# Performance work log

Hardware: AMD Instinct MI355X
Metric: run time of the kernel (lower is better)

## Reference

```python
import jax, jax.numpy as jnp
import numpy as np

B, S, D = 32, 512, 512      # batch, seq_len, d_model
H, K = 16, 32               # head_num, head_dim
A = 256                     # attention_hidden_dim


def setup_inputs() -> dict:
    key = jax.random.key(0)
    ks = jax.random.split(key, 10)
    s = lambda fan_in: 1.0 / np.sqrt(fan_in)
    return {
        "x":   jax.random.normal(ks[0], (B, S, D), dtype=jnp.float32),
        # per-head Q projections: Linear(D, D), stored [H, in, out]
        "Qw":  jax.random.normal(ks[1], (H, D, D), dtype=jnp.float32) * s(D),
        "Qb":  jax.random.normal(ks[2], (H, D), dtype=jnp.float32) * s(D),
        # per-head V projections: Linear(D, K)
        "Vw":  jax.random.normal(ks[3], (H, D, K), dtype=jnp.float32) * s(D),
        "Vb":  jax.random.normal(ks[4], (H, K), dtype=jnp.float32) * s(D),
        # additive attention pooling: Linear(H*K, A) then Linear(A, 1)
        "Wv":  jax.random.normal(ks[5], (H * K, A), dtype=jnp.float32) * s(H * K),
        "bv":  jax.random.normal(ks[6], (A,), dtype=jnp.float32) * s(H * K),
        "wq":  jax.random.normal(ks[7], (A, 1), dtype=jnp.float32) * s(A),
        "bq":  jax.random.normal(ks[8], (1,), dtype=jnp.float32) * s(A),
    }


def reference(x, Qw, Qb, Vw, Vb, Wv, bv, wq, bq):
    # per-head query projection: [B, H, S, D]
    q = jnp.einsum("bsd,hde->bhse", x, Qw) + Qb[None, :, None, :]
    # raw scores: [B, H, S, S] (s = query pos, t = key pos)
    scores = jnp.einsum("bhse,bte->bhst", q, x)
    # NOTE: softmax over dim=-2 (the QUERY axis), not the usual key axis
    attn = jax.nn.softmax(scores, axis=-2)
    # context: [B, H, S, D]
    ctx = jnp.einsum("bhst,btd->bhsd", attn, x)
    # per-head value projection then concat heads -> [B, S, H*K]
    head_out = jnp.einsum("bhsd,hdk->bshk", ctx, Vw) + Vb[None, None, :, :]
    h = head_out.reshape(B, S, H * K)
    # dropout is identity at inference
    # additive attention pooling
    a = jnp.tanh(h @ Wv + bv) @ wq + bq          # [B, S, 1]
    z = jnp.einsum("bs,bsk->bk", a[..., 0], h)   # [B, H*K]
    return z
```

## Files before the change

kernel.cpp:

```cpp
#include <hip/hip_runtime.h>

#define DEVFN __device__ __forceinline__

typedef _Float16 f16;
typedef _Float16 f16x8 __attribute__((ext_vector_type(8)));
typedef _Float16 f16x4 __attribute__((ext_vector_type(4)));
typedef float    f32x4 __attribute__((ext_vector_type(4)));

enum { NB = 32, NS = 512, ND = 512, NH = 16, NK = 32, NA = 256 };

#define SZ(x) ((size_t)(x))

typedef __attribute__((address_space(3))) void       as3_void;
typedef const __attribute__((address_space(1))) void as1_cvoid;
DEVFN void ldsdma16(const void* g, void* l) {
  __builtin_amdgcn_global_load_lds((as1_cvoid*)g, (as3_void*)l, 16, 0, 0);
}

DEVFN void gemm_core_128(const f16* __restrict__ Ag, const f16* __restrict__ Bg,
                         int lda, int ldb, int nk, f16* lds, f32x4 acc[4][4]) {
  f16* As = lds;
  f16* Bs = lds + 128 * 64;
  const int tid  = threadIdx.x;
  const int lane = tid & 63;
  const int wvid = tid >> 6, wr = wvid >> 1, wc = wvid & 1;
  const int srow = tid >> 3, scol = (tid & 7) * 8;
  const int frow = lane & 15, fk = (lane >> 4) * 8;
  for (int ks = 0; ks < nk; ++ks) {
    const f16* ga = Ag + ks * 64 + scol;
    const f16* gb = Bg + ks * 64 + scol;
#pragma unroll
    for (int r = 0; r < 4; ++r) {
      ldsdma16(ga + SZ(r * 32 + srow) * lda, As + SZ(r * 32 + srow) * 64 + scol);
      ldsdma16(gb + SZ(r * 32 + srow) * ldb, Bs + SZ(r * 32 + srow) * 64 + scol);
    }
    __syncthreads();
#pragma unroll
    for (int kk = 0; kk < 64; kk += 32) {
      f16x8 a[4], b[4];
#pragma unroll
      for (int i = 0; i < 4; ++i)
        a[i] = *(const f16x8*)(As + SZ(wr * 64 + i * 16 + frow) * 64 + kk + fk);
#pragma unroll
      for (int j = 0; j < 4; ++j)
        b[j] = *(const f16x8*)(Bs + SZ(wc * 64 + j * 16 + frow) * 64 + kk + fk);
#pragma unroll
      for (int i = 0; i < 4; ++i)
#pragma unroll
        for (int j = 0; j < 4; ++j)
          acc[i][j] = __builtin_amdgcn_mfma_f32_16x16x32_f16(a[i], b[j], acc[i][j], 0, 0, 0);
    }
    __syncthreads();
  }
}

DEVFN void wlds_write(f16* wlds, int row, int col, f16 v) {
  int byte = (row * 256 + col * 2) ^ ((row & 7) << 4);
  *(f16*)((char*)wlds + byte) = v;
}
DEVFN f16x8 wlds_read8(const f16* wlds, int row, int col ) {
  int byte = (row * 256 + col * 2) ^ ((row & 7) << 4);
  return *(const f16x8*)((const char*)wlds + byte);
}

__global__ __launch_bounds__(256) void k_cast4(const float* __restrict__ s,
                                               f16* __restrict__ d, int n4) {
  int i = blockIdx.x * 256 + threadIdx.x;
  if (i >= n4) return;
  float4 v = ((const float4*)s)[i];
  f16x4 o; o[0] = (f16)v.x; o[1] = (f16)v.y; o[2] = (f16)v.z; o[3] = (f16)v.w;
  ((f16x4*)d)[i] = o;
}

__global__ void k_tcast(const float* __restrict__ src, f16* __restrict__ dst,
                        int R, int C, long sStride, long dStride) {
  __shared__ float tile[32][33];
  src += (long)blockIdx.z * sStride;
  dst += (long)blockIdx.z * dStride;
  int c0 = blockIdx.x * 32, r0 = blockIdx.y * 32;
  int tx = threadIdx.x, ty = threadIdx.y;
#pragma unroll
  for (int i = 0; i < 4; ++i)
    tile[ty + 8 * i][tx] = src[(long)(r0 + ty + 8 * i) * C + c0 + tx];
  __syncthreads();
#pragma unroll
  for (int i = 0; i < 4; ++i)
    dst[(long)(c0 + ty + 8 * i) * R + r0 + tx] = (f16)tile[tx][ty + 8 * i];
}

__global__ __launch_bounds__(256) void k_gemm_xv(const f16* __restrict__ xh,
                                                 const f16* __restrict__ vwt,
                                                 f16* __restrict__ xvt) {
  __shared__ f16 smem[128 * 64 * 2];
  int z = blockIdx.z, b = z >> 2, hg = z & 3, tm = blockIdx.x;
  f32x4 acc[4][4] = {};
  gemm_core_128(xh + SZ(b) * NS * ND + SZ(tm) * 128 * ND,
                vwt + SZ(hg) * 4 * NK * ND, ND, ND, ND / 64, smem, acc);
  int tid = threadIdx.x, lane = tid & 63, wvid = tid >> 6, wr = wvid >> 1, wc = wvid & 1;
  int rbase = (lane >> 4) * 4, cbase = lane & 15;
#pragma unroll
  for (int mi = 0; mi < 4; ++mi)
#pragma unroll
    for (int ni = 0; ni < 4; ++ni) {
      int n = wc * 64 + ni * 16 + cbase;
      int hh = hg * 4 + (n >> 5), kk = n & 31;
#pragma unroll
      for (int r = 0; r < 4; ++r) {
        int t = tm * 128 + wr * 64 + mi * 16 + rbase + r;
        xvt[(SZ(b * NH + hh) * NK + kk) * NS + t] = (f16)acc[mi][ni][r];
      }
    }
}

__global__ __launch_bounds__(256) void k_gemm_q(const f16* __restrict__ xh,
                                                const f16* __restrict__ qwt,
                                                const float* __restrict__ Qb,
                                                f16* __restrict__ qc, int b0) {
  __shared__ f16 smem[128 * 64 * 2];
  int bhl = blockIdx.z, b = b0 + (bhl >> 4), h = bhl & 15;
  int tm = blockIdx.x, tn = blockIdx.y;
  f32x4 acc[4][4] = {};
  gemm_core_128(xh + SZ(b) * NS * ND + SZ(tm) * 128 * ND,
                qwt + SZ(h) * ND * ND + SZ(tn) * 128 * ND, ND, ND, ND / 64, smem, acc);
  int tid = threadIdx.x, lane = tid & 63, wvid = tid >> 6, wr = wvid >> 1, wc = wvid & 1;
  int rbase = (lane >> 4) * 4, cbase = lane & 15;
  f16* qb = qc + SZ(bhl) * NS * ND;
#pragma unroll
  for (int mi = 0; mi < 4; ++mi)
#pragma unroll
    for (int ni = 0; ni < 4; ++ni) {
      int colg = tn * 128 + wc * 64 + ni * 16 + cbase;
      float bias = Qb[h * ND + colg];
#pragma unroll
      for (int r = 0; r < 4; ++r) {
        int rowg = tm * 128 + wr * 64 + mi * 16 + rbase + r;
        qb[SZ(rowg) * ND + colg] = (f16)(acc[mi][ni][r] + bias);
      }
    }
}

__global__ __launch_bounds__(256) void k_scores_stats(const f16* __restrict__ qc,
                                                      const f16* __restrict__ xh,
                                                      f16* __restrict__ sc,
                                                      float* __restrict__ mp,
                                                      float* __restrict__ zp, int b0) {
  __shared__ f16 smem[128 * 64 * 2];
  int bhl = blockIdx.z, b = b0 + (bhl >> 4);
  int st = blockIdx.x, tt = blockIdx.y;
  f32x4 acc[4][4] = {};
  gemm_core_128(qc + SZ(bhl) * NS * ND + SZ(st) * 128 * ND,
                xh + SZ(b) * NS * ND + SZ(tt) * 128 * ND, ND, ND, ND / 64, smem, acc);
  int tid = threadIdx.x, lane = tid & 63, wvid = tid >> 6, wr = wvid >> 1, wc = wvid & 1;
  f16* scb = sc + (SZ(bhl * 4 + st) * 4 + tt) * (128 * 128);
#pragma unroll
  for (int mi = 0; mi < 4; ++mi)
#pragma unroll
    for (int ni = 0; ni < 4; ++ni) {
      f16x4 o;
#pragma unroll
      for (int r = 0; r < 4; ++r) o[r] = (f16)acc[mi][ni][r];
      ((f16x4*)(scb + (mi * 4 + ni) * 1024))[tid] = o;
    }
  float mx[4], sm[4];
#pragma unroll
  for (int ni = 0; ni < 4; ++ni) {
    float m = -1e30f;
#pragma unroll
    for (int mi = 0; mi < 4; ++mi)
#pragma unroll
      for (int r = 0; r < 4; ++r) m = fmaxf(m, acc[mi][ni][r]);
    m = fmaxf(m, __shfl_xor(m, 16));
    m = fmaxf(m, __shfl_xor(m, 32));
    float s = 0.f;
#pragma unroll
    for (int mi = 0; mi < 4; ++mi)
#pragma unroll
      for (int r = 0; r < 4; ++r) s += __expf(acc[mi][ni][r] - m);
    s += __shfl_xor(s, 16);
    s += __shfl_xor(s, 32);
    mx[ni] = m; sm[ni] = s;
  }
  float2* sbuf = (float2*)smem;
  if (lane < 16) {
#pragma unroll
    for (int ni = 0; ni < 4; ++ni)
      sbuf[wr * 128 + wc * 64 + ni * 16 + lane] = make_float2(mx[ni], sm[ni]);
  }
  __syncthreads();
  if (tid < 128) {
    float2 p0 = sbuf[tid], p1 = sbuf[128 + tid];
    float m = fmaxf(p0.x, p1.x);
    float zz = p0.y * __expf(p0.x - m) + p1.y * __expf(p1.x - m);
    size_t idx = (SZ(bhl) * 4 + st) * NS + tt * 128 + tid;
    mp[idx] = m; zp[idx] = zz;
  }
}

__global__ __launch_bounds__(256) void k_stats_combine(const float* __restrict__ mp,
                                                       const float* __restrict__ zp,
                                                       float* __restrict__ mf,
                                                       float* __restrict__ rz) {
  int i = blockIdx.x * 256 + threadIdx.x;
  int bhl = i >> 9, t = i & (NS - 1);
  float mv[4], m = -1e30f;
#pragma unroll
  for (int st = 0; st < 4; ++st) {
    mv[st] = mp[(SZ(bhl) * 4 + st) * NS + t];
    m = fmaxf(m, mv[st]);
  }
  float z = 0.f;
#pragma unroll
  for (int st = 0; st < 4; ++st) z += zp[(SZ(bhl) * 4 + st) * NS + t] * __expf(mv[st] - m);
  mf[i] = m; rz[i] = 1.0f / z;
}

__global__ __launch_bounds__(256) void k_norm_pv(const f16* __restrict__ sc,
                                                 const f16* __restrict__ xvt,
                                                 const float* __restrict__ mf,
                                                 const float* __restrict__ rz,
                                                 const float* __restrict__ Vb,
                                                 f16* __restrict__ h16, int b0) {
  __shared__ f16 wlds[128 * 128];
  int bhl = blockIdx.y, b = b0 + (bhl >> 4), h = bhl & 15;
  int st = blockIdx.x;
  int tid = threadIdx.x, lane = tid & 63, wvid = tid >> 6, wr = wvid >> 1, wc = wvid & 1;
  int rbase = (lane >> 4) * 4, cbase = lane & 15, fk = (lane >> 4) * 8;
  f32x4 acc2[2][2] = {};
  const f16* xvh = xvt + SZ(b * NH + h) * NK * NS;
  for (int tt = 0; tt < 4; ++tt) {
    const f16* scb = sc + (SZ(bhl * 4 + st) * 4 + tt) * (128 * 128);
#pragma unroll
    for (int ni = 0; ni < 4; ++ni) {
      int tl = wc * 64 + ni * 16 + cbase;
      int tg = tt * 128 + tl;
      float mv = mf[SZ(bhl) * NS + tg], rzv = rz[SZ(bhl) * NS + tg];
#pragma unroll
      for (int mi = 0; mi < 4; ++mi) {
        f16x4 v = ((const f16x4*)(scb + (mi * 4 + ni) * 1024))[tid];
#pragma unroll
        for (int r = 0; r < 4; ++r) {
          int sl = wr * 64 + mi * 16 + rbase + r;
          wlds_write(wlds, sl, tl, (f16)(__expf((float)v[r] - mv) * rzv));
        }
      }
    }
    __syncthreads();
    const f16* xvb = xvh + tt * 128;
#pragma unroll
    for (int tc = 0; tc < 4; ++tc) {
      f16x8 aw[2], bx[2];
#pragma unroll
      for (int m2 = 0; m2 < 2; ++m2)
        aw[m2] = wlds_read8(wlds, wvid * 32 + m2 * 16 + cbase, tc * 32 + fk);
#pragma unroll
      for (int n2 = 0; n2 < 2; ++n2)
        bx[n2] = *(const f16x8*)(xvb + SZ(n2 * 16 + cbase) * NS + tc * 32 + fk);
#pragma unroll
      for (int m2 = 0; m2 < 2; ++m2)
#pragma unroll
        for (int n2 = 0; n2 < 2; ++n2)
          acc2[m2][n2] = __builtin_amdgcn_mfma_f32_16x16x32_f16(aw[m2], bx[n2], acc2[m2][n2], 0, 0, 0);
    }
    __syncthreads();
  }
  const float* vb = Vb + h * NK;
#pragma unroll
  for (int m2 = 0; m2 < 2; ++m2)
#pragma unroll
    for (int n2 = 0; n2 < 2; ++n2)
#pragma unroll
      for (int r = 0; r < 4; ++r) {
        int sg = st * 128 + wvid * 32 + m2 * 16 + rbase + r;
        int kk = n2 * 16 + cbase;
        float val = acc2[m2][n2][r] + vb[kk];
        h16[SZ(b * NS + sg) * (NH * NK) + h * NK + kk] = (f16)val;
      }
}

__global__ __launch_bounds__(256) void k_gemm_u(const f16* __restrict__ h16,
                                                const f16* __restrict__ wvt,
                                                const float* __restrict__ bv,
                                                f16* __restrict__ U) {
  __shared__ f16 smem[128 * 64 * 2];
  int tm = blockIdx.x, tn = blockIdx.y;
  f32x4 acc[4][4] = {};
  gemm_core_128(h16 + SZ(tm) * 128 * ND, wvt + SZ(tn) * 128 * ND, ND, ND, ND / 64, smem, acc);
  int tid = threadIdx.x, lane = tid & 63, wvid = tid >> 6, wr = wvid >> 1, wc = wvid & 1;
  int rbase = (lane >> 4) * 4, cbase = lane & 15;
#pragma unroll
  for (int mi = 0; mi < 4; ++mi)
#pragma unroll
    for (int ni = 0; ni < 4; ++ni) {
      int colg = tn * 128 + wc * 64 + ni * 16 + cbase;
      float bias = bv[colg];
#pragma unroll
      for (int r = 0; r < 4; ++r) {
        int rowg = tm * 128 + wr * 64 + mi * 16 + rbase + r;
        U[SZ(rowg) * NA + colg] = (f16)tanhf(acc[mi][ni][r] + bias);
      }
    }
}

__global__ __launch_bounds__(256) void k_a(const f16* __restrict__ U,
                                           const float* __restrict__ wq,
                                           const float* __restrict__ bq,
                                           float* __restrict__ a) {
  int wid = (blockIdx.x * 256 + threadIdx.x) >> 6;
  int lane = threadIdx.x & 63;
  const f16* u = U + SZ(wid) * NA;
  float p = 0.f;
#pragma unroll
  for (int j = 0; j < NA / 64; ++j) p += (float)u[lane + 64 * j] * wq[lane + 64 * j];
#pragma unroll
  for (int o = 32; o; o >>= 1) p += __shfl_xor(p, o);
  if (lane == 0) a[wid] = p + bq[0];
}

__global__ __launch_bounds__(256) void k_zpart(const f16* __restrict__ h16,
                                               const float* __restrict__ a,
                                               float* __restrict__ zpt) {
  int b = blockIdx.y, c = blockIdx.x, tid = threadIdx.x;
  float z0 = 0.f, z1 = 0.f;
  for (int s = 0; s < 64; ++s) {
    int sg = c * 64 + s;
    float av = a[b * NS + sg];
    const f16* hr = h16 + SZ(b * NS + sg) * (NH * NK);
    z0 += av * (float)hr[tid];
    z1 += av * (float)hr[tid + 256];
  }
  zpt[SZ(b * 8 + c) * 512 + tid] = z0;
  zpt[SZ(b * 8 + c) * 512 + tid + 256] = z1;
}

__global__ __launch_bounds__(256) void k_zred(const float* __restrict__ zpt,
                                              float* __restrict__ out) {
  int i = blockIdx.x * 256 + threadIdx.x;
  int b = i >> 9, k = i & 511;
  float z = 0.f;
#pragma unroll
  for (int c = 0; c < 8; ++c) z += zpt[SZ(b * 8 + c) * 512 + k];
  out[i] = z;
}

static size_t ws_plan(int cb, size_t off[15]) {
  size_t o = 0;
  auto put = [&](size_t bytes) { size_t r = o; o += (bytes + 255) & ~SZ(255); return r; };
  off[0]  = put(SZ(NB) * NS * ND * 2);
  off[1]  = put(SZ(NH) * ND * ND * 2);
  off[2]  = put(SZ(NA) * ND * 2);
  off[3]  = put(SZ(NH) * NK * ND * 2);
  off[4]  = put(SZ(NB) * NH * NK * NS * 2);
  off[5]  = put(SZ(cb) * NH * NS * ND * 2);
  off[6]  = put(SZ(cb) * NH * NS * NS * 2);
  off[7]  = put(SZ(cb) * NH * 4 * NS * 4);
  off[8]  = put(SZ(cb) * NH * 4 * NS * 4);
  off[9]  = put(SZ(cb) * NH * NS * 4);
  off[10] = put(SZ(cb) * NH * NS * 4);
  off[11] = put(SZ(NB) * NS * NH * NK * 2);
  off[12] = put(SZ(NB) * NS * NA * 2);
  off[13] = put(SZ(NB) * NS * 4);
  off[14] = put(SZ(NB) * 8 * NH * NK * 4);
  return o;
}

extern "C" void kernel_launch(void* const* d_in, const int* in_sizes, int n_in,
                              void* d_out, int out_size, void* d_ws, size_t ws_size,
                              hipStream_t stream) {
  const float* x  = (const float*)d_in[0];
  const float* Qw = (const float*)d_in[1];
  const float* Qb = (const float*)d_in[2];
  const float* Vw = (const float*)d_in[3];
  const float* Vb = (const float*)d_in[4];
  const float* Wv = (const float*)d_in[5];
  const float* bv = (const float*)d_in[6];
  const float* wq = (const float*)d_in[7];
  const float* bq = (const float*)d_in[8];

  int cbv = 0;
  size_t off[15];
  const int cand[5] = {32, 16, 8, 4, 2};
  for (int ci = 0; ci < 5; ++ci) {
    if (ws_plan(cand[ci], off) <= ws_size) { cbv = cand[ci]; break; }
  }
  if (cbv == 0) return;

  char* ws = (char*)d_ws;
  f16*   xh   = (f16*)(ws + off[0]);
  f16*   qwt  = (f16*)(ws + off[1]);
  f16*   wvt  = (f16*)(ws + off[2]);
  f16*   vwt  = (f16*)(ws + off[3]);
  f16*   xvt  = (f16*)(ws + off[4]);
  f16*   qc   = (f16*)(ws + off[5]);
  f16*   sc   = (f16*)(ws + off[6]);
  float* mp   = (float*)(ws + off[7]);
  float* zps  = (float*)(ws + off[8]);
  float* mf   = (float*)(ws + off[9]);
  float* rz   = (float*)(ws + off[10]);
  f16*   h16  = (f16*)(ws + off[11]);
  f16*   U    = (f16*)(ws + off[12]);
  float* a    = (float*)(ws + off[13]);
  float* zpt  = (float*)(ws + off[14]);
  float* zout = (float*)d_out;

  k_cast4<<<SZ(NB) * NS * ND / 4 / 256, 256, 0, stream>>>(x, xh, NB * NS * ND / 4);
  k_tcast<<<dim3(16, 16, 16), dim3(32, 8), 0, stream>>>(Qw, qwt, ND, ND, (long)ND * ND, (long)ND * ND);
  k_tcast<<<dim3(8, 16, 1), dim3(32, 8), 0, stream>>>(Wv, wvt, ND, NA, 0, 0);
  k_tcast<<<dim3(1, 16, 16), dim3(32, 8), 0, stream>>>(Vw, vwt, ND, NK, (long)ND * NK, (long)NK * ND);
  k_gemm_xv<<<dim3(4, 1, NB * 4), 256, 0, stream>>>(xh, vwt, xvt);

  for (int b0 = 0; b0 < NB; b0 += cbv) {
    k_gemm_q<<<dim3(4, 4, cbv * NH), 256, 0, stream>>>(xh, qwt, Qb, qc, b0);
    k_scores_stats<<<dim3(4, 4, cbv * NH), 256, 0, stream>>>(qc, xh, sc, mp, zps, b0);
    k_stats_combine<<<cbv * NH * NS / 256, 256, 0, stream>>>(mp, zps, mf, rz);
    k_norm_pv<<<dim3(4, cbv * NH), 256, 0, stream>>>(sc, xvt, mf, rz, Vb, h16, b0);
  }

  k_gemm_u<<<dim3(NB * NS / 128, 2, 1), 256, 0, stream>>>(h16, wvt, bv, U);
  k_a<<<NB * NS / 4, 256, 0, stream>>>(U, wq, bq, a);
  k_zpart<<<dim3(8, NB), 256, 0, stream>>>(h16, a, zpt);
  k_zred<<<NB * 512 / 256, 256, 0, stream>>>(zpt, zout);
}
```

Baseline: 612.9 us.

## Store exponentiated scores, precompute per-tile softmax scales, swizzle blocks across XCDs

The scores kernel now reduces the column max across the tile first, then writes exp(score - tile max) as f16 instead of raw scores. The combine kernel emits one scale per (query tile, key) pair, so the normalize/PV kernel does a single multiply instead of an exp per element. GEMM blocks in the Q and scores kernels are remapped with an XCD-aware swizzle so tiles that share inputs land on the same chiplet's cache, and the z-partial loop reads f16 pairs. This adds an extra barrier and LDS round-trip in the scores kernel. Storing exponentials in f16 instead of raw scores changes rounding behaviour.

```diff
diff --git a/kernel.cpp b/kernel.cpp
--- a/kernel.cpp
+++ b/kernel.cpp
@@ -5,6 +5,7 @@
 typedef _Float16 f16;
 typedef _Float16 f16x8 __attribute__((ext_vector_type(8)));
 typedef _Float16 f16x4 __attribute__((ext_vector_type(4)));
+typedef _Float16 f16x2 __attribute__((ext_vector_type(2)));
 typedef float    f32x4 __attribute__((ext_vector_type(4)));
 
 enum { NB = 32, NS = 512, ND = 512, NH = 16, NK = 32, NA = 256 };
@@ -15,6 +16,10 @@
 typedef const __attribute__((address_space(1))) void as1_cvoid;
 DEVFN void ldsdma16(const void* g, void* l) {
   __builtin_amdgcn_global_load_lds((as1_cvoid*)g, (as3_void*)l, 16, 0, 0);
+}
+
+DEVFN int xcd_swz(int flat, int n) {
+  return (flat & 7) * (n >> 3) + (flat >> 3);
 }
 
 DEVFN void gemm_core_128(const f16* __restrict__ Ag, const f16* __restrict__ Bg,
@@ -117,8 +122,11 @@
                                                 const float* __restrict__ Qb,
                                                 f16* __restrict__ qc, int b0) {
   __shared__ f16 smem[128 * 64 * 2];
-  int bhl = blockIdx.z, b = b0 + (bhl >> 4), h = bhl & 15;
-  int tm = blockIdx.x, tn = blockIdx.y;
+  int n = gridDim.x * gridDim.y * gridDim.z;
+  int flat = blockIdx.x + gridDim.x * (blockIdx.y + gridDim.y * blockIdx.z);
+  int lg = xcd_swz(flat, n);
+  int tm = lg & 3, tn = (lg >> 2) & 3, bhl = lg >> 4;
+  int b = b0 + (bhl >> 4), h = bhl & 15;
   f32x4 acc[4][4] = {};
   gemm_core_128(xh + SZ(b) * NS * ND + SZ(tm) * 128 * ND,
                 qwt + SZ(h) * ND * ND + SZ(tn) * 128 * ND, ND, ND, ND / 64, smem, acc);
@@ -145,23 +153,18 @@
                                                       float* __restrict__ mp,
                                                       float* __restrict__ zp, int b0) {
   __shared__ f16 smem[128 * 64 * 2];
-  int bhl = blockIdx.z, b = b0 + (bhl >> 4);
-  int st = blockIdx.x, tt = blockIdx.y;
+  int n = gridDim.x * gridDim.y * gridDim.z;
+  int flat = blockIdx.x + gridDim.x * (blockIdx.y + gridDim.y * blockIdx.z);
+  int lg = xcd_swz(flat, n);
+  int st = lg & 3, tt = (lg >> 2) & 3, bhl = lg >> 4;
+  int b = b0 + (bhl >> 4);
   f32x4 acc[4][4] = {};
   gemm_core_128(qc + SZ(bhl) * NS * ND + SZ(st) * 128 * ND,
                 xh + SZ(b) * NS * ND + SZ(tt) * 128 * ND, ND, ND, ND / 64, smem, acc);
   int tid = threadIdx.x, lane = tid & 63, wvid = tid >> 6, wr = wvid >> 1, wc = wvid & 1;
-  f16* scb = sc + (SZ(bhl * 4 + st) * 4 + tt) * (128 * 128);
-#pragma unroll
-  for (int mi = 0; mi < 4; ++mi)
-#pragma unroll
-    for (int ni = 0; ni < 4; ++ni) {
-      f16x4 o;
-#pragma unroll
-      for (int r = 0; r < 4; ++r) o[r] = (f16)acc[mi][ni][r];
-      ((f16x4*)(scb + (mi * 4 + ni) * 1024))[tid] = o;
-    }
-  float mx[4], sm[4];
+  float* sbuf = (float*)smem;
+
+  float mh[4];
 #pragma unroll
   for (int ni = 0; ni < 4; ++ni) {
     float m = -1e30f;
@@ -171,26 +174,53 @@
       for (int r = 0; r < 4; ++r) m = fmaxf(m, acc[mi][ni][r]);
     m = fmaxf(m, __shfl_xor(m, 16));
     m = fmaxf(m, __shfl_xor(m, 32));
-    float s = 0.f;
-#pragma unroll
-    for (int mi = 0; mi < 4; ++mi)
-#pragma unroll
-      for (int r = 0; r < 4; ++r) s += __expf(acc[mi][ni][r] - m);
-    s += __shfl_xor(s, 16);
-    s += __shfl_xor(s, 32);
-    mx[ni] = m; sm[ni] = s;
-  }
-  float2* sbuf = (float2*)smem;
+    mh[ni] = m;
+  }
   if (lane < 16) {
 #pragma unroll
     for (int ni = 0; ni < 4; ++ni)
-      sbuf[wr * 128 + wc * 64 + ni * 16 + lane] = make_float2(mx[ni], sm[ni]);
+      sbuf[wr * 128 + wc * 64 + ni * 16 + lane] = mh[ni];
+  }
+  __syncthreads();
+  int cbase = lane & 15;
+  float tmc[4];
+#pragma unroll
+  for (int ni = 0; ni < 4; ++ni) {
+    int col = wc * 64 + ni * 16 + cbase;
+    tmc[ni] = fmaxf(sbuf[col], sbuf[128 + col]);
+  }
+  f16* scb = sc + (SZ(bhl * 4 + st) * 4 + tt) * (128 * 128);
+  float sm[4];
+#pragma unroll
+  for (int ni = 0; ni < 4; ++ni) sm[ni] = 0.f;
+#pragma unroll
+  for (int mi = 0; mi < 4; ++mi) {
+#pragma unroll
+    for (int ni = 0; ni < 4; ++ni) {
+      f16x4 o;
+#pragma unroll
+      for (int r = 0; r < 4; ++r) {
+        float ev = __expf(acc[mi][ni][r] - tmc[ni]);
+        o[r] = (f16)ev;
+        sm[ni] += ev;
+      }
+      ((f16x4*)(scb + (mi * 4 + ni) * 1024))[tid] = o;
+    }
+  }
+#pragma unroll
+  for (int ni = 0; ni < 4; ++ni) {
+    sm[ni] += __shfl_xor(sm[ni], 16);
+    sm[ni] += __shfl_xor(sm[ni], 32);
+  }
+  if (lane < 16) {
+#pragma unroll
+    for (int ni = 0; ni < 4; ++ni)
+      sbuf[256 + wr * 128 + wc * 64 + ni * 16 + lane] = sm[ni];
   }
   __syncthreads();
   if (tid < 128) {
-    float2 p0 = sbuf[tid], p1 = sbuf[128 + tid];
-    float m = fmaxf(p0.x, p1.x);
-    float zz = p0.y * __expf(p0.x - m) + p1.y * __expf(p1.x - m);
+    float m  = fmaxf(sbuf[tid], sbuf[128 + tid]);
+    float zz = sbuf[256 + tid] + sbuf[384 + tid];
     size_t idx = (SZ(bhl) * 4 + st) * NS + tt * 128 + tid;
     mp[idx] = m; zp[idx] = zz;
   }
@@ -198,8 +228,7 @@
 
 __global__ __launch_bounds__(256) void k_stats_combine(const float* __restrict__ mp,
                                                        const float* __restrict__ zp,
-                                                       float* __restrict__ mf,
-                                                       float* __restrict__ rz) {
+                                                       float* __restrict__ cs) {
   int i = blockIdx.x * 256 + threadIdx.x;
   int bhl = i >> 9, t = i & (NS - 1);
   float mv[4], m = -1e30f;
@@ -208,16 +237,21 @@
     mv[st] = mp[(SZ(bhl) * 4 + st) * NS + t];
     m = fmaxf(m, mv[st]);
   }
-  float z = 0.f;
-#pragma unroll
-  for (int st = 0; st < 4; ++st) z += zp[(SZ(bhl) * 4 + st) * NS + t] * __expf(mv[st] - m);
-  mf[i] = m; rz[i] = 1.0f / z;
+  float es[4], Z = 0.f;
+#pragma unroll
+  for (int st = 0; st < 4; ++st) {
+    es[st] = __expf(mv[st] - m);
+    Z += zp[(SZ(bhl) * 4 + st) * NS + t] * es[st];
+  }
+  float rZ = 1.0f / Z;
+#pragma unroll
+  for (int st = 0; st < 4; ++st)
+    cs[(SZ(bhl) * 4 + st) * NS + t] = es[st] * rZ;
 }
 
 __global__ __launch_bounds__(256) void k_norm_pv(const f16* __restrict__ sc,
                                                  const f16* __restrict__ xvt,
-                                                 const float* __restrict__ mf,
-                                                 const float* __restrict__ rz,
+                                                 const float* __restrict__ cs,
                                                  const float* __restrict__ Vb,
                                                  f16* __restrict__ h16, int b0) {
   __shared__ f16 wlds[128 * 128];
@@ -232,15 +266,14 @@
 #pragma unroll
     for (int ni = 0; ni < 4; ++ni) {
       int tl = wc * 64 + ni * 16 + cbase;
-      int tg = tt * 128 + tl;
-      float mv = mf[SZ(bhl) * NS + tg], rzv = rz[SZ(bhl) * NS + tg];
+      float csv = cs[(SZ(bhl) * 4 + st) * NS + tt * 128 + tl];
 #pragma unroll
       for (int mi = 0; mi < 4; ++mi) {
         f16x4 v = ((const f16x4*)(scb + (mi * 4 + ni) * 1024))[tid];
 #pragma unroll
         for (int r = 0; r < 4; ++r) {
           int sl = wr * 64 + mi * 16 + rbase + r;
-          wlds_write(wlds, sl, tl, (f16)(__expf((float)v[r] - mv) * rzv));
+          wlds_write(wlds, sl, tl, (f16)((float)v[r] * csv));
         }
       }
     }
@@ -325,11 +358,12 @@
     int sg = c * 64 + s;
     float av = a[b * NS + sg];
     const f16* hr = h16 + SZ(b * NS + sg) * (NH * NK);
-    z0 += av * (float)hr[tid];
-    z1 += av * (float)hr[tid + 256];
-  }
-  zpt[SZ(b * 8 + c) * 512 + tid] = z0;
-  zpt[SZ(b * 8 + c) * 512 + tid + 256] = z1;
+    f16x2 v = ((const f16x2*)hr)[tid];
+    z0 += av * (float)v[0];
+    z1 += av * (float)v[1];
+  }
+  zpt[SZ(b * 8 + c) * 512 + 2 * tid]     = z0;
+  zpt[SZ(b * 8 + c) * 512 + 2 * tid + 1] = z1;
 }
 
 __global__ __launch_bounds__(256) void k_zred(const float* __restrict__ zpt,
@@ -342,7 +376,7 @@
   out[i] = z;
 }
 
-static size_t ws_plan(int cb, size_t off[15]) {
+static size_t ws_plan(int cb, size_t off[14]) {
   size_t o = 0;
   auto put = [&](size_t bytes) { size_t r = o; o += (bytes + 255) & ~SZ(255); return r; };
   off[0]  = put(SZ(NB) * NS * ND * 2);
@@ -354,12 +388,11 @@
   off[6]  = put(SZ(cb) * NH * NS * NS * 2);
   off[7]  = put(SZ(cb) * NH * 4 * NS * 4);
   off[8]  = put(SZ(cb) * NH * 4 * NS * 4);
-  off[9]  = put(SZ(cb) * NH * NS * 4);
-  off[10] = put(SZ(cb) * NH * NS * 4);
-  off[11] = put(SZ(NB) * NS * NH * NK * 2);
-  off[12] = put(SZ(NB) * NS * NA * 2);
-  off[13] = put(SZ(NB) * NS * 4);
-  off[14] = put(SZ(NB) * 8 * NH * NK * 4);
+  off[9]  = put(SZ(cb) * NH * 4 * NS * 4);
+  off[10] = put(SZ(NB) * NS * NH * NK * 2);
+  off[11] = put(SZ(NB) * NS * NA * 2);
+  off[12] = put(SZ(NB) * NS * 4);
+  off[13] = put(SZ(NB) * 8 * NH * NK * 4);
   return o;
 }
 
@@ -377,7 +410,7 @@
   const float* bq = (const float*)d_in[8];
 
   int cbv = 0;
-  size_t off[15];
+  size_t off[14];
   const int cand[5] = {32, 16, 8, 4, 2};
   for (int ci = 0; ci < 5; ++ci) {
     if (ws_plan(cand[ci], off) <= ws_size) { cbv = cand[ci]; break; }
@@ -394,12 +427,11 @@
   f16*   sc   = (f16*)(ws + off[6]);
   float* mp   = (float*)(ws + off[7]);
   float* zps  = (float*)(ws + off[8]);
-  float* mf   = (float*)(ws + off[9]);
-  float* rz   = (float*)(ws + off[10]);
-  f16*   h16  = (f16*)(ws + off[11]);
-  f16*   U    = (f16*)(ws + off[12]);
-  float* a    = (float*)(ws + off[13]);
-  float* zpt  = (float*)(ws + off[14]);
+  float* cs   = (float*)(ws + off[9]);
+  f16*   h16  = (f16*)(ws + off[10]);
+  f16*   U    = (f16*)(ws + off[11]);
+  float* a    = (float*)(ws + off[12]);
+  float* zpt  = (float*)(ws + off[13]);
   float* zout = (float*)d_out;
 
   k_cast4<<<SZ(NB) * NS * ND / 4 / 256, 256, 0, stream>>>(x, xh, NB * NS * ND / 4);
@@ -411,8 +443,8 @@
   for (int b0 = 0; b0 < NB; b0 += cbv) {
     k_gemm_q<<<dim3(4, 4, cbv * NH), 256, 0, stream>>>(xh, qwt, Qb, qc, b0);
     k_scores_stats<<<dim3(4, 4, cbv * NH), 256, 0, stream>>>(qc, xh, sc, mp, zps, b0);
-    k_stats_combine<<<cbv * NH * NS / 256, 256, 0, stream>>>(mp, zps, mf, rz);
-    k_norm_pv<<<dim3(4, cbv * NH), 256, 0, stream>>>(sc, xvt, mf, rz, Vb, h16, b0);
+    k_stats_combine<<<cbv * NH * NS / 256, 256, 0, stream>>>(mp, zps, cs);
+    k_norm_pv<<<dim3(4, cbv * NH), 256, 0, stream>>>(sc, xvt, cs, Vb, h16, b0);
   }
 
   k_gemm_u<<<dim3(NB * NS / 128, 2, 1), 256, 0, stream>>>(h16, wvt, bv, U);
```

Result: faster. 573.5 us (-6.4%).
